# Kernel optimization log

Hardware: AMD Instinct MI355X
Metric: run time of the kernel (lower is better)

The kernel has to match this reference:

```python
import jax, jax.numpy as jnp
import numpy as np

NUM_HEADS = 32
NUM_KV_HEADS = 8
HEAD_DIM = 128


def rotate_half(x):
    half = x.shape[-1] // 2
    return jnp.concatenate([-x[..., half:], x[..., :half]], axis=-1)


def setup_inputs() -> dict:
    key = jax.random.key(0)
    ks = jax.random.split(key, 7)
    B, S, H = 2, 2048, 4096
    hidden_states = jax.random.normal(ks[0], (B, S, H), dtype=jnp.float32)
    # rope tables built from real frequencies for realism
    inv_freq = 1.0 / (10000.0 ** (jnp.arange(0, HEAD_DIM, 2, dtype=jnp.float32) / HEAD_DIM))
    pos = jnp.arange(S, dtype=jnp.float32)
    freqs = pos[:, None] * inv_freq[None, :]            # [S, HEAD_DIM//2]
    emb = jnp.concatenate([freqs, freqs], axis=-1)      # [S, HEAD_DIM]
    cos = jnp.broadcast_to(jnp.cos(emb)[None], (B, S, HEAD_DIM)).astype(jnp.float32)
    sin = jnp.broadcast_to(jnp.sin(emb)[None], (B, S, HEAD_DIM)).astype(jnp.float32)
    scale = 0.02
    wq = jax.random.normal(ks[1], (NUM_HEADS * HEAD_DIM, H), dtype=jnp.float32) * scale
    wk = jax.random.normal(ks[2], (NUM_KV_HEADS * HEAD_DIM, H), dtype=jnp.float32) * scale
    wv = jax.random.normal(ks[3], (NUM_KV_HEADS * HEAD_DIM, H), dtype=jnp.float32) * scale
    wo = jax.random.normal(ks[4], (H, NUM_HEADS * HEAD_DIM), dtype=jnp.float32) * scale
    return {"hidden_states": hidden_states, "cos": cos, "sin": sin,
            "wq": wq, "wk": wk, "wv": wv, "wo": wo}


def reference(hidden_states, cos, sin, wq, wk, wv, wo):
    B, S, H = hidden_states.shape
    groups = NUM_HEADS // NUM_KV_HEADS
    scaling = HEAD_DIM ** -0.5

    # QKV projections (nn.Linear, no bias -> x @ W^T)
    q = (hidden_states @ wq.T).reshape(B, S, NUM_HEADS, HEAD_DIM).transpose(0, 2, 1, 3)     # [B,Hq,S,D]
    k = (hidden_states @ wk.T).reshape(B, S, NUM_KV_HEADS, HEAD_DIM).transpose(0, 2, 1, 3)  # [B,Hk,S,D]
    v = (hidden_states @ wv.T).reshape(B, S, NUM_KV_HEADS, HEAD_DIM).transpose(0, 2, 1, 3)  # [B,Hk,S,D]

    # RoPE (HF apply_rotary_pos_emb: cos/sin unsqueezed over head axis)
    c = cos[:, None, :, :]  # [B,1,S,D]
    s = sin[:, None, :, :]
    q = q * c + rotate_half(q) * s
    k = k * c + rotate_half(k) * s

    # GQA: broadcast each KV head to its group of query heads
    k = jnp.repeat(k, groups, axis=1)  # [B,Hq,S,D]
    v = jnp.repeat(v, groups, axis=1)

    # causal SDPA
    scores = jnp.einsum('bhqd,bhkd->bhqk', q, k) * scaling
    causal = jnp.tril(jnp.ones((S, S), dtype=bool))
    neg = jnp.finfo(scores.dtype).min
    scores = jnp.where(causal[None, None], scores, neg)
    probs = jax.nn.softmax(scores, axis=-1)
    attn = jnp.einsum('bhqk,bhkd->bhqd', probs, v)      # [B,Hq,S,D]

    # merge heads + output projection
    attn = attn.transpose(0, 2, 1, 3).reshape(B, S, NUM_HEADS * HEAD_DIM)
    return attn @ wo.T
```

## Files before the change

### kernel.cpp

```cpp
#include <hip/hip_runtime.h>
#include <stdint.h>

typedef __bf16 bf16_t;
typedef __bf16 bf16x8 __attribute__((ext_vector_type(8)));
typedef __bf16 bf16x4 __attribute__((ext_vector_type(4)));
typedef float f32x4 __attribute__((ext_vector_type(4)));

#define S_LEN 2048
#define NH 32
#define NKV 8
#define HD 128
#define B_SZ 2
#define HID 4096
#define QKV_N 6144
#define INFF __builtin_inff()

__device__ __forceinline__ void gload_lds16(const void* g, void* l) {
    __builtin_amdgcn_global_load_lds(
        (const __attribute__((address_space(1))) void*)(uintptr_t)g,
        (__attribute__((address_space(3))) void*)(uint32_t)(uintptr_t)l,
        16, 0, 0);
}

__global__ __launch_bounds__(256) void f2b_kernel(const float4* __restrict__ in,
                                                  bf16x4* __restrict__ out, int n4) {
    int i = blockIdx.x * blockDim.x + threadIdx.x;
    if (i >= n4) return;
    float4 v = in[i];
    bf16x4 o = {(bf16_t)v.x, (bf16_t)v.y, (bf16_t)v.z, (bf16_t)v.w};
    out[i] = o;
}

#define SLOT_E 16384

#define GTILE(T, STAGE, VMW) do {                                                         \
    const int _sb = ((T) & 3) * SLOT_E;                                                   \
    bf16x8 af[8], bfr[2];                                                                 \
    _Pragma("unroll") for (int i = 0; i < 8; ++i)                                         \
        af[i] = *(const bf16x8*)&lds[_sb + offA[i]];                                      \
    bfr[0] = *(const bf16x8*)&lds[_sb + 8192 + offB[0]];                                  \
    bfr[1] = *(const bf16x8*)&lds[_sb + 8192 + offB[1]];                                  \
    if (STAGE) {                                                                          \
        const int _ss = (((T) + 3) & 3) * SLOT_E;                                         \
        gload_lds16(sA0, &lds[_ss + ldsO0]); gload_lds16(sA1, &lds[_ss + ldsO1]);         \
        sA0 += 32; sA1 += 32;                                                             \
    }                                                                                     \
    __builtin_amdgcn_s_barrier();                                                         \
    asm volatile("s_waitcnt lgkmcnt(0)" ::: "memory");                                    \
    __builtin_amdgcn_sched_barrier(0);                                                    \
    __builtin_amdgcn_s_setprio(1);                                                        \
    _Pragma("unroll") for (int i = 0; i < 8; ++i) {                                       \
        acc[i][0] = __builtin_amdgcn_mfma_f32_16x16x32_bf16(af[i], bfr[0], acc[i][0], 0, 0, 0); \
        acc[i][1] = __builtin_amdgcn_mfma_f32_16x16x32_bf16(af[i], bfr[1], acc[i][1], 0, 0, 0); \
    }                                                                                     \
    __builtin_amdgcn_s_setprio(0);                                                        \
    __builtin_amdgcn_s_barrier();                                                         \
    bf16x8 bfs[2];                                                                        \
    bfs[0] = *(const bf16x8*)&lds[_sb + 8192 + offB[2]];                                  \
    bfs[1] = *(const bf16x8*)&lds[_sb + 8192 + offB[3]];                                  \
    if (STAGE) {                                                                          \
        const int _ss = (((T) + 3) & 3) * SLOT_E;                                         \
        gload_lds16(sB0, &lds[_ss + 8192 + ldsO0]); gload_lds16(sB1, &lds[_ss + 8192 + ldsO1]); \
        sB0 += 32; sB1 += 32;                                                             \
    }                                                                                     \
    __builtin_amdgcn_s_barrier();                                                         \
    asm volatile("s_waitcnt lgkmcnt(0)" ::: "memory");                                    \
    __builtin_amdgcn_sched_barrier(0);                                                    \
    __builtin_amdgcn_s_setprio(1);                                                        \
    _Pragma("unroll") for (int i = 0; i < 8; ++i) {                                       \
        acc[i][2] = __builtin_amdgcn_mfma_f32_16x16x32_bf16(af[i], bfs[0], acc[i][2], 0, 0, 0); \
        acc[i][3] = __builtin_amdgcn_mfma_f32_16x16x32_bf16(af[i], bfs[1], acc[i][3], 0, 0, 0); \
    }                                                                                     \
    __builtin_amdgcn_s_setprio(0);                                                        \
    if ((VMW) == 8)      asm volatile("s_waitcnt vmcnt(8)" ::: "memory");                 \
    else if ((VMW) == 4) asm volatile("s_waitcnt vmcnt(4)" ::: "memory");                 \
    else if ((VMW) == 0) asm volatile("s_waitcnt vmcnt(0)" ::: "memory");                 \
    __builtin_amdgcn_s_barrier();                                                         \
} while (0)

template<bool F32OUT>
__global__ __launch_bounds__(512, 2) void gemm256(const bf16_t* __restrict__ A,
                                                  const bf16_t* __restrict__ W,
                                                  void* __restrict__ Cv,
                                                  int M, int N, int K) {
    __shared__ __align__(16) bf16_t lds[4 * SLOT_E];
    const int tid = threadIdx.x;
    const int lane = tid & 63;
    const int w = tid >> 6;
    const int wm = w >> 2, wn = w & 3;
    const int l15 = lane & 15, lg = lane >> 4;

    const int nbx = N >> 8;
    const int cpx = gridDim.x >> 3;
    const int bid = blockIdx.x;
    const int bid2 = (bid & 7) * cpx + (bid >> 3);
    const int m0 = (bid2 / nbx) * 256;
    const int n0 = (bid2 % nbx) * 256;

    const int c0 = tid, c1 = 512 + tid;
    const int rA0 = c0 >> 2, ch0 = (c0 & 3) ^ ((rA0 >> 1) & 3);
    const int rA1 = c1 >> 2, ch1 = (c1 & 3) ^ ((rA1 >> 1) & 3);
    const bf16_t* sA0 = A + (size_t)(m0 + rA0) * K + ch0 * 8;
    const bf16_t* sA1 = A + (size_t)(m0 + rA1) * K + ch1 * 8;
    const bf16_t* sB0 = W + (size_t)(n0 + rA0) * K + ch0 * 8;
    const bf16_t* sB1 = W + (size_t)(n0 + rA1) * K + ch1 * 8;
    const int ldsO0 = c0 * 8, ldsO1 = c1 * 8;

    int offA[8], offB[4];
    #pragma unroll
    for (int i = 0; i < 8; ++i) {
        int row = wm * 128 + i * 16 + l15;
        offA[i] = row * 32 + ((lg ^ ((row >> 1) & 3)) * 8);
    }
    #pragma unroll
    for (int j = 0; j < 4; ++j) {
        int row = wn * 64 + j * 16 + l15;
        offB[j] = row * 32 + ((lg ^ ((row >> 1) & 3)) * 8);
    }

    #pragma unroll
    for (int tt = 0; tt < 3; ++tt) {
        const int ss = tt * SLOT_E;
        gload_lds16(sA0, &lds[ss + ldsO0]); gload_lds16(sA1, &lds[ss + ldsO1]);
        gload_lds16(sB0, &lds[ss + 8192 + ldsO0]); gload_lds16(sB1, &lds[ss + 8192 + ldsO1]);
        sA0 += 32; sA1 += 32; sB0 += 32; sB1 += 32;
    }
    asm volatile("s_waitcnt vmcnt(8)" ::: "memory");
    __builtin_amdgcn_s_barrier();

    f32x4 acc[8][4] = {};
    const int NT = K >> 5;
    int t = 0;
    for (; t < NT - 3; ++t) GTILE(t, true, 8);
    GTILE(NT - 3, false, 4);
    GTILE(NT - 2, false, 0);
    GTILE(NT - 1, false, -1);

    #pragma unroll
    for (int i = 0; i < 8; ++i)
        #pragma unroll
        for (int jn = 0; jn < 4; ++jn)
            #pragma unroll
            for (int r = 0; r < 4; ++r) {
                int m = m0 + wm * 128 + i * 16 + lg * 4 + r;
                int n = n0 + wn * 64 + jn * 16 + l15;
                float v = acc[i][jn][r];
                if (F32OUT) ((float*)Cv)[(size_t)m * N + n] = v;
                else        ((bf16_t*)Cv)[(size_t)m * N + n] = (bf16_t)v;
            }
}

__global__ __launch_bounds__(256) void rope_kernel(bf16_t* __restrict__ QKV,
                                                   const float* __restrict__ cosb,
                                                   const float* __restrict__ sinb) {
    int tid = blockIdx.x * blockDim.x + threadIdx.x;
    int d = tid & 63;
    int h40 = (tid >> 6) % (NH + NKV);
    int bs = tid / (64 * (NH + NKV));
    int col = (h40 < NH) ? h40 * HD : HID + (h40 - NH) * HD;
    bf16_t* rowp = QKV + (size_t)bs * QKV_N + col;
    float x1 = (float)rowp[d];
    float x2 = (float)rowp[d + 64];
    float c1 = cosb[(size_t)bs * HD + d];
    float s1 = sinb[(size_t)bs * HD + d];
    float c2 = cosb[(size_t)bs * HD + d + 64];
    float s2 = sinb[(size_t)bs * HD + d + 64];
    rowp[d]      = (bf16_t)(x1 * c1 - x2 * s1);
    rowp[d + 64] = (bf16_t)(x2 * c2 + x1 * s2);
}

#define PITCH_P 72

__global__ __launch_bounds__(256, 3) void attn_fwd(const bf16_t* __restrict__ QKV,
                                                   bf16_t* __restrict__ O) {
    __shared__ __align__(16) bf16_t Kl[64 * 128];
    __shared__ __align__(16) bf16_t Vt[128 * 64];
    __shared__ __align__(16) bf16_t Pl[4][16 * PITCH_P];
    const int tid = threadIdx.x;
    const int lane = tid & 63;
    const int w = tid >> 6;
    const int l15 = lane & 15, lg = lane >> 4;
    const int pr = blockIdx.x, h = blockIdx.y, b = blockIdx.z;
    const int kvh = h >> 2;
    const float scale = 0.08838834764831845f;

    int krow[4], kch[4];
    for (int jj = 0; jj < 4; ++jj) { int q = jj * 256 + tid; krow[jj] = q >> 4; kch[jj] = q & 15; }
    const int d0 = (tid >> 4) * 8;
    const int k0v = (tid & 15) * 4;
    const int vci = k0v >> 3;
    const int vsub = k0v & 7;

    const bf16_t* Kb0 = QKV + (size_t)(b * S_LEN) * QKV_N + HID + kvh * HD;
    const bf16_t* Vb0 = QKV + (size_t)(b * S_LEN) * QKV_N + HID + NKV * HD + kvh * HD;
    bf16_t* Plw = Pl[w];

    for (int t = 0; t < 2; ++t) {
        const int qt = (t == 0) ? pr : (31 - pr);
        const int q0 = qt * 64;
        const int qrow = q0 + w * 16 + l15;

        bf16x8 qf[4];
        {
            const bf16_t* qp = QKV + (size_t)(b * S_LEN + qrow) * QKV_N + h * HD;
            for (int c = 0; c < 4; ++c) qf[c] = *(const bf16x8*)&qp[c * 32 + lg * 8];
        }

        f32x4 acc_o[8] = {};
        float mrow = -INFF, lrow = 0.f;
        const int nsteps = qt + 1;

        bf16x8 kst[4], vst[4];
        for (int jj = 0; jj < 4; ++jj)
            kst[jj] = *(const bf16x8*)&Kb0[(size_t)krow[jj] * QKV_N + kch[jj] * 8];
        for (int j2 = 0; j2 < 4; ++j2)
            vst[j2] = *(const bf16x8*)&Vb0[(size_t)(k0v + j2) * QKV_N + d0];

        for (int st = 0; st < nsteps; ++st) {
            const int k0 = st * 64;
            __syncthreads();
            for (int jj = 0; jj < 4; ++jj)
                *(bf16x8*)&Kl[krow[jj] * 128 + ((kch[jj] ^ (krow[jj] & 7)) * 8)] = kst[jj];
            #pragma unroll
            for (int j = 0; j < 8; ++j) {
                bf16x4 cvec = { vst[0][j], vst[1][j], vst[2][j], vst[3][j] };
                *(bf16x4*)&Vt[(d0 + j) * 64 + ((vci ^ j) << 3) + vsub] = cvec;
            }
            __syncthreads();
            if (st + 1 < nsteps) {
                const bf16_t* Kb = Kb0 + (size_t)(k0 + 64) * QKV_N;
                const bf16_t* Vb = Vb0 + (size_t)(k0 + 64) * QKV_N;
                for (int jj = 0; jj < 4; ++jj)
                    kst[jj] = *(const bf16x8*)&Kb[(size_t)krow[jj] * QKV_N + kch[jj] * 8];
                for (int j2 = 0; j2 < 4; ++j2)
                    vst[j2] = *(const bf16x8*)&Vb[(size_t)(k0v + j2) * QKV_N + d0];
            }
            f32x4 s[4];
            #pragma unroll
            for (int nt = 0; nt < 4; ++nt) {
                s[nt] = (f32x4){0.f, 0.f, 0.f, 0.f};
                const int row = nt * 16 + l15;
                const int rb = row * 128, key = row & 7;
                #pragma unroll
                for (int c = 0; c < 4; ++c) {
                    bf16x8 kf = *(const bf16x8*)&Kl[rb + (((c * 4 + lg) ^ key) * 8)];
                    s[nt] = __builtin_amdgcn_mfma_f32_16x16x32_bf16(kf, qf[c], s[nt], 0, 0, 0);
                }
            }
            float ev[4][4];
            float mx = -INFF;
            #pragma unroll
            for (int nt = 0; nt < 4; ++nt)
                #pragma unroll
                for (int r = 0; r < 4; ++r) {
                    int k = k0 + nt * 16 + lg * 4 + r;
                    float v = (k <= qrow) ? s[nt][r] * scale : -INFF;
                    ev[nt][r] = v;
                    mx = fmaxf(mx, v);
                }
            mx = fmaxf(mx, __shfl_xor(mx, 16));
            mx = fmaxf(mx, __shfl_xor(mx, 32));
            const float mn = fmaxf(mrow, mx);
            const float sc = __expf(mrow - mn);
            float rs = 0.f;
            #pragma unroll
            for (int nt = 0; nt < 4; ++nt)
                #pragma unroll
                for (int r = 0; r < 4; ++r) {
                    float e = __expf(ev[nt][r] - mn);
                    ev[nt][r] = e; rs += e;
                }
            rs += __shfl_xor(rs, 16);
            rs += __shfl_xor(rs, 32);
            mrow = mn;
            lrow = lrow * sc + rs;
            #pragma unroll
            for (int nt = 0; nt < 4; ++nt) {
                bf16x4 pk = {(bf16_t)ev[nt][0], (bf16_t)ev[nt][1], (bf16_t)ev[nt][2], (bf16_t)ev[nt][3]};
                *(bf16x4*)&Plw[l15 * PITCH_P + nt * 16 + lg * 4] = pk;
            }
            float scb[4];
            #pragma unroll
            for (int r = 0; r < 4; ++r) scb[r] = __shfl(sc, lg * 4 + r);
            #pragma unroll
            for (int nt2 = 0; nt2 < 8; ++nt2)
                #pragma unroll
                for (int r = 0; r < 4; ++r) acc_o[nt2][r] *= scb[r];
            #pragma unroll
            for (int kc = 0; kc < 2; ++kc) {
                bf16x8 pf = *(const bf16x8*)&Plw[l15 * PITCH_P + kc * 32 + lg * 8];
                #pragma unroll
                for (int nt2 = 0; nt2 < 8; ++nt2) {
                    const int drow = nt2 * 16 + l15;
                    bf16x8 vf = *(const bf16x8*)&Vt[drow * 64 + (((kc * 4 + lg) ^ (drow & 7)) << 3)];
                    acc_o[nt2] = __builtin_amdgcn_mfma_f32_16x16x32_bf16(pf, vf, acc_o[nt2], 0, 0, 0);
                }
            }
        }
        float lb[4];
        #pragma unroll
        for (int r = 0; r < 4; ++r) lb[r] = __shfl(lrow, lg * 4 + r);
        #pragma unroll
        for (int nt2 = 0; nt2 < 8; ++nt2)
            #pragma unroll
            for (int r = 0; r < 4; ++r) {
                int q = q0 + w * 16 + lg * 4 + r;
                int d = nt2 * 16 + l15;
                O[((size_t)(b * S_LEN + q)) * (NH * HD) + h * HD + d] = (bf16_t)(acc_o[nt2][r] / lb[r]);
            }
    }
}

extern "C" void kernel_launch(void* const* d_in, const int* in_sizes, int n_in,
                              void* d_out, int out_size, void* d_ws, size_t ws_size,
                              hipStream_t stream) {
    const float* hs   = (const float*)d_in[0];
    const float* cosb = (const float*)d_in[1];
    const float* sinb = (const float*)d_in[2];
    const float* wq   = (const float*)d_in[3];
    const float* wk   = (const float*)d_in[4];
    const float* wv   = (const float*)d_in[5];
    const float* wo   = (const float*)d_in[6];
    float* out = (float*)d_out;

    const size_t NHS = (size_t)B_SZ * S_LEN * HID;
    const size_t NQKVW = (size_t)QKV_N * HID;
    size_t need = (NHS * 3 + NQKVW * 2) * sizeof(bf16_t);
    if (ws_size < need) return;

    bf16_t* p = (bf16_t*)d_ws;
    bf16_t* hsb  = p; p += NHS;
    bf16_t* wqkv = p; p += NQKVW;
    bf16_t* wob  = p; p += NHS;
    bf16_t* QKVb = p; p += NQKVW;
    bf16_t* Ab   = p; p += NHS;

    auto cvt = [&](const float* src, bf16_t* dst, size_t n) {
        int n4 = (int)(n / 4);
        f2b_kernel<<<(n4 + 255) / 256, 256, 0, stream>>>((const float4*)src, (bf16x4*)dst, n4);
    };
    cvt(hs, hsb, NHS);
    cvt(wq, wqkv, NHS);
    cvt(wk, wqkv + (size_t)HID * HID, (size_t)NKV * HD * HID);
    cvt(wv, wqkv + (size_t)(HID + NKV * HD) * HID, (size_t)NKV * HD * HID);
    cvt(wo, wob, NHS);

    const int M = B_SZ * S_LEN;
    gemm256<false><<<(M / 256) * (QKV_N / 256), 512, 0, stream>>>(hsb, wqkv, QKVb, M, QKV_N, HID);

    int rope_threads = B_SZ * S_LEN * (NH + NKV) * 64;
    rope_kernel<<<rope_threads / 256, 256, 0, stream>>>(QKVb, cosb, sinb);

    attn_fwd<<<dim3(16, NH, B_SZ), 256, 0, stream>>>(QKVb, Ab);

    gemm256<true><<<(M / 256) * (HID / 256), 512, 0, stream>>>(Ab, wob, out, M, HID, HID);
}
```

Before: 592.1 us.

## Split-K the KV projection, fuse partial sum into RoPE, double-buffer attention LDS

The QKV GEMM is split into a Q GEMM and a KV GEMM. The KV GEMM uses split-K across two grid slices, with the second partial written to a scratch buffer, so the small N=2048 launch fills more CUs. The RoPE kernel now also adds the split-K partials for K and V. Attention double-buffers its K/V LDS tiles to drop one barrier per step, lowers occupancy to 2 blocks, and defers softmax rescaling when the running max grows by at most 8. The risks are extra partial-sum traffic, lower attention occupancy, and bf16 rounding of the split partials.

```diff
diff --git a/kernel.cpp b/kernel.cpp
--- a/kernel.cpp
+++ b/kernel.cpp
@@ -81,8 +81,10 @@
 template<bool F32OUT>
 __global__ __launch_bounds__(512, 2) void gemm256(const bf16_t* __restrict__ A,
                                                   const bf16_t* __restrict__ W,
-                                                  void* __restrict__ Cv,
-                                                  int M, int N, int K) {
+                                                  void* __restrict__ C0,
+                                                  void* __restrict__ C1,
+                                                  int ld0, int ld1,
+                                                  int Nloc, int ldAW, int Kloc) {
     __shared__ __align__(16) bf16_t lds[4 * SLOT_E];
     const int tid = threadIdx.x;
     const int lane = tid & 63;
@@ -90,7 +92,12 @@
     const int wm = w >> 2, wn = w & 3;
     const int l15 = lane & 15, lg = lane >> 4;
 
-    const int nbx = N >> 8;
+    const int z = blockIdx.y;
+    void* Cv = z ? C1 : C0;
+    const int ldC = z ? ld1 : ld0;
+    const int kOff = z * Kloc;
+
+    const int nbx = Nloc >> 8;
     const int cpx = gridDim.x >> 3;
     const int bid = blockIdx.x;
     const int bid2 = (bid & 7) * cpx + (bid >> 3);
@@ -100,10 +107,10 @@
     const int c0 = tid, c1 = 512 + tid;
     const int rA0 = c0 >> 2, ch0 = (c0 & 3) ^ ((rA0 >> 1) & 3);
     const int rA1 = c1 >> 2, ch1 = (c1 & 3) ^ ((rA1 >> 1) & 3);
-    const bf16_t* sA0 = A + (size_t)(m0 + rA0) * K + ch0 * 8;
-    const bf16_t* sA1 = A + (size_t)(m0 + rA1) * K + ch1 * 8;
-    const bf16_t* sB0 = W + (size_t)(n0 + rA0) * K + ch0 * 8;
-    const bf16_t* sB1 = W + (size_t)(n0 + rA1) * K + ch1 * 8;
+    const bf16_t* sA0 = A + (size_t)(m0 + rA0) * ldAW + kOff + ch0 * 8;
+    const bf16_t* sA1 = A + (size_t)(m0 + rA1) * ldAW + kOff + ch1 * 8;
+    const bf16_t* sB0 = W + (size_t)(n0 + rA0) * ldAW + kOff + ch0 * 8;
+    const bf16_t* sB1 = W + (size_t)(n0 + rA1) * ldAW + kOff + ch1 * 8;
     const int ldsO0 = c0 * 8, ldsO1 = c1 * 8;
 
     int offA[8], offB[4];
@@ -129,7 +136,7 @@
     __builtin_amdgcn_s_barrier();
 
     f32x4 acc[8][4] = {};
-    const int NT = K >> 5;
+    const int NT = Kloc >> 5;
     int t = 0;
     for (; t < NT - 3; ++t) GTILE(t, true, 8);
     GTILE(NT - 3, false, 4);
@@ -145,22 +152,39 @@
                 int m = m0 + wm * 128 + i * 16 + lg * 4 + r;
                 int n = n0 + wn * 64 + jn * 16 + l15;
                 float v = acc[i][jn][r];
-                if (F32OUT) ((float*)Cv)[(size_t)m * N + n] = v;
-                else        ((bf16_t*)Cv)[(size_t)m * N + n] = (bf16_t)v;
-            }
-}
-
-__global__ __launch_bounds__(256) void rope_kernel(bf16_t* __restrict__ QKV,
-                                                   const float* __restrict__ cosb,
-                                                   const float* __restrict__ sinb) {
+                if (F32OUT) ((float*)Cv)[(size_t)m * ldC + n] = v;
+                else        ((bf16_t*)Cv)[(size_t)m * ldC + n] = (bf16_t)v;
+            }
+}
+
+__global__ __launch_bounds__(256) void rope_fuse(bf16_t* __restrict__ QKV,
+                                                 const bf16_t* __restrict__ P1,
+                                                 const float* __restrict__ cosb,
+                                                 const float* __restrict__ sinb) {
     int tid = blockIdx.x * blockDim.x + threadIdx.x;
     int d = tid & 63;
-    int h40 = (tid >> 6) % (NH + NKV);
-    int bs = tid / (64 * (NH + NKV));
-    int col = (h40 < NH) ? h40 * HD : HID + (h40 - NH) * HD;
-    bf16_t* rowp = QKV + (size_t)bs * QKV_N + col;
-    float x1 = (float)rowp[d];
-    float x2 = (float)rowp[d + 64];
+    int hg = (tid >> 6) % 48;
+    int bs = tid / (64 * 48);
+    bf16_t* rowp;
+    float x1, x2;
+    if (hg < 32) {
+        rowp = QKV + (size_t)bs * QKV_N + hg * HD;
+        x1 = (float)rowp[d];
+        x2 = (float)rowp[d + 64];
+    } else if (hg < 40) {
+        int col = HID + (hg - 32) * HD;
+        rowp = QKV + (size_t)bs * QKV_N + col;
+        const bf16_t* pp = P1 + (size_t)bs * 2048 + (col - HID);
+        x1 = (float)rowp[d] + (float)pp[d];
+        x2 = (float)rowp[d + 64] + (float)pp[d + 64];
+    } else {
+        int col = HID + NKV * HD + (hg - 40) * HD;
+        rowp = QKV + (size_t)bs * QKV_N + col;
+        const bf16_t* pp = P1 + (size_t)bs * 2048 + (col - HID);
+        rowp[d]      = (bf16_t)((float)rowp[d]      + (float)pp[d]);
+        rowp[d + 64] = (bf16_t)((float)rowp[d + 64] + (float)pp[d + 64]);
+        return;
+    }
     float c1 = cosb[(size_t)bs * HD + d];
     float s1 = sinb[(size_t)bs * HD + d];
     float c2 = cosb[(size_t)bs * HD + d + 64];
@@ -171,10 +195,10 @@
 
 #define PITCH_P 72
 
-__global__ __launch_bounds__(256, 3) void attn_fwd(const bf16_t* __restrict__ QKV,
+__global__ __launch_bounds__(256, 2) void attn_fwd(const bf16_t* __restrict__ QKV,
                                                    bf16_t* __restrict__ O) {
-    __shared__ __align__(16) bf16_t Kl[64 * 128];
-    __shared__ __align__(16) bf16_t Vt[128 * 64];
+    __shared__ __align__(16) bf16_t Kl[2][64 * 128];
+    __shared__ __align__(16) bf16_t Vt[2][128 * 64];
     __shared__ __align__(16) bf16_t Pl[4][16 * PITCH_P];
     const int tid = threadIdx.x;
     const int lane = tid & 63;
@@ -216,15 +240,17 @@
         for (int j2 = 0; j2 < 4; ++j2)
             vst[j2] = *(const bf16x8*)&Vb0[(size_t)(k0v + j2) * QKV_N + d0];
 
+        __syncthreads();
+
         for (int st = 0; st < nsteps; ++st) {
             const int k0 = st * 64;
-            __syncthreads();
+            const int p = st & 1;
             for (int jj = 0; jj < 4; ++jj)
-                *(bf16x8*)&Kl[krow[jj] * 128 + ((kch[jj] ^ (krow[jj] & 7)) * 8)] = kst[jj];
+                *(bf16x8*)&Kl[p][krow[jj] * 128 + ((kch[jj] ^ (krow[jj] & 7)) * 8)] = kst[jj];
             #pragma unroll
             for (int j = 0; j < 8; ++j) {
                 bf16x4 cvec = { vst[0][j], vst[1][j], vst[2][j], vst[3][j] };
-                *(bf16x4*)&Vt[(d0 + j) * 64 + ((vci ^ j) << 3) + vsub] = cvec;
+                *(bf16x4*)&Vt[p][(d0 + j) * 64 + ((vci ^ j) << 3) + vsub] = cvec;
             }
             __syncthreads();
             if (st + 1 < nsteps) {
@@ -243,7 +269,7 @@
                 const int rb = row * 128, key = row & 7;
                 #pragma unroll
                 for (int c = 0; c < 4; ++c) {
-                    bf16x8 kf = *(const bf16x8*)&Kl[rb + (((c * 4 + lg) ^ key) * 8)];
+                    bf16x8 kf = *(const bf16x8*)&Kl[p][rb + (((c * 4 + lg) ^ key) * 8)];
                     s[nt] = __builtin_amdgcn_mfma_f32_16x16x32_bf16(kf, qf[c], s[nt], 0, 0, 0);
                 }
             }
@@ -260,8 +286,10 @@
                 }
             mx = fmaxf(mx, __shfl_xor(mx, 16));
             mx = fmaxf(mx, __shfl_xor(mx, 32));
-            const float mn = fmaxf(mrow, mx);
-            const float sc = __expf(mrow - mn);
+            const bool nodefer = !__all(mx <= mrow + 8.f);
+            float mn, sc;
+            if (nodefer) { mn = fmaxf(mrow, mx); sc = __expf(mrow - mn); }
+            else         { mn = mrow;            sc = 1.f; }
             float rs = 0.f;
             #pragma unroll
             for (int nt = 0; nt < 4; ++nt)
@@ -279,20 +307,22 @@
                 bf16x4 pk = {(bf16_t)ev[nt][0], (bf16_t)ev[nt][1], (bf16_t)ev[nt][2], (bf16_t)ev[nt][3]};
                 *(bf16x4*)&Plw[l15 * PITCH_P + nt * 16 + lg * 4] = pk;
             }
-            float scb[4];
-            #pragma unroll
-            for (int r = 0; r < 4; ++r) scb[r] = __shfl(sc, lg * 4 + r);
-            #pragma unroll
-            for (int nt2 = 0; nt2 < 8; ++nt2)
-                #pragma unroll
-                for (int r = 0; r < 4; ++r) acc_o[nt2][r] *= scb[r];
+            if (nodefer) {
+                float scb[4];
+                #pragma unroll
+                for (int r = 0; r < 4; ++r) scb[r] = __shfl(sc, lg * 4 + r);
+                #pragma unroll
+                for (int nt2 = 0; nt2 < 8; ++nt2)
+                    #pragma unroll
+                    for (int r = 0; r < 4; ++r) acc_o[nt2][r] *= scb[r];
+            }
             #pragma unroll
             for (int kc = 0; kc < 2; ++kc) {
                 bf16x8 pf = *(const bf16x8*)&Plw[l15 * PITCH_P + kc * 32 + lg * 8];
                 #pragma unroll
                 for (int nt2 = 0; nt2 < 8; ++nt2) {
                     const int drow = nt2 * 16 + l15;
-                    bf16x8 vf = *(const bf16x8*)&Vt[drow * 64 + (((kc * 4 + lg) ^ (drow & 7)) << 3)];
+                    bf16x8 vf = *(const bf16x8*)&Vt[p][drow * 64 + (((kc * 4 + lg) ^ (drow & 7)) << 3)];
                     acc_o[nt2] = __builtin_amdgcn_mfma_f32_16x16x32_bf16(pf, vf, acc_o[nt2], 0, 0, 0);
                 }
             }
@@ -334,6 +364,7 @@
     bf16_t* wob  = p; p += NHS;
     bf16_t* QKVb = p; p += NQKVW;
     bf16_t* Ab   = p; p += NHS;
+    bf16_t* P1   = Ab;
 
     auto cvt = [&](const float* src, bf16_t* dst, size_t n) {
         int n4 = (int)(n / 4);
@@ -345,13 +376,17 @@
     cvt(wv, wqkv + (size_t)(HID + NKV * HD) * HID, (size_t)NKV * HD * HID);
     cvt(wo, wob, NHS);
 
-    const int M = B_SZ * S_LEN;
-    gemm256<false><<<(M / 256) * (QKV_N / 256), 512, 0, stream>>>(hsb, wqkv, QKVb, M, QKV_N, HID);
-
-    int rope_threads = B_SZ * S_LEN * (NH + NKV) * 64;
-    rope_kernel<<<rope_threads / 256, 256, 0, stream>>>(QKVb, cosb, sinb);
+    gemm256<false><<<dim3(256, 1), 512, 0, stream>>>(hsb, wqkv, QKVb, QKVb,
+                                                     QKV_N, QKV_N, 4096, HID, HID);
+    gemm256<false><<<dim3(128, 2), 512, 0, stream>>>(hsb, wqkv + (size_t)HID * HID,
+                                                     QKVb + HID, P1,
+                                                     QKV_N, 2048, 2048, HID, 2048);
+
+    int rf_threads = B_SZ * S_LEN * 48 * 64;
+    rope_fuse<<<rf_threads / 256, 256, 0, stream>>>(QKVb, P1, cosb, sinb);
 
     attn_fwd<<<dim3(16, NH, B_SZ), 256, 0, stream>>>(QKVb, Ab);
 
-    gemm256<true><<<(M / 256) * (HID / 256), 512, 0, stream>>>(Ab, wob, out, M, HID, HID);
-}
+    gemm256<true><<<dim3(256, 1), 512, 0, stream>>>(Ab, wob, out, out,
+                                                    HID, HID, HID, HID, HID);
+}
```

Result: faster. 563.7 us (-4.8%).
